# Kernel optimization log

Hardware: AMD Instinct MI355X
Metric: run time of the kernel (lower is better)

## Reference

```python
import jax, jax.numpy as jnp
import numpy as np

# Correlation hyperparameters (from init_kwargs):
PAD = 4            # pad_size
KERNEL = 1         # kernel_size (point-wise)
MD = 4             # max_displacement
STRIDE1 = 1
STRIDE2 = 1

B, C, H, W = 8, 256, 96, 160


def setup_inputs() -> dict:
    key = jax.random.key(0)
    k1, k2 = jax.random.split(key)
    input1 = jax.random.normal(k1, (B, C, H, W), dtype=jnp.float32)
    input2 = jax.random.normal(k2, (B, C, H, W), dtype=jnp.float32)
    return {"input1": input1, "input2": input2}


def reference(input1, input2):
    """FlowNet-style correlation cost volume.

    out[b, (dy+MD)*D + (dx+MD), y, x] = (1/C) * sum_c in1[b,c,y,x] * in2pad[b,c,y+dy+PAD, x+dx+PAD]
    where in2pad is input2 zero-padded by PAD and D = 2*MD+1. With PAD == MD,
    kernel_size == 1, stride1 == stride2 == 1 the output is [B, D*D, H, W].
    """
    b, c, h, w = input1.shape
    in2p = jnp.pad(input2, ((0, 0), (0, 0), (PAD, PAD), (PAD, PAD)))
    D = 2 * MD + 1
    outs = []
    # Fixed small 81-iteration loop over displacements (not a data dim).
    for dy in range(0, 2 * MD + 1, STRIDE2):
        for dx in range(0, 2 * MD + 1, STRIDE2):
            shifted = jax.lax.dynamic_slice(in2p, (0, 0, dy, dx), (b, c, h, w))
            # mean over channels == sum / (kernel^2 * C) with kernel == 1
            outs.append(jnp.mean(input1 * shifted, axis=1))
    return jnp.stack(outs, axis=1)  # [B, 81, H, W]
```

## Files before the change

### kernel.cpp

```cpp
#include <hip/hip_runtime.h>
#include <stdint.h>

#define B_ 8
#define C_ 256
#define H_ 96
#define W_ 160
#define ND 9
#define NDISP 81
#define NCHUNK 128
#define TX 4
#define NXG 20
#define NTHR 256
#define NCOMP 180
#define IN2_OFF 320
#define ROW_B 352
#define BUF_B 3584
#define NBUF 4
#define NSEG 218
#define HW (H_ * W_)
#define CHSTEP (2 * HW)

typedef __attribute__((ext_vector_type(2))) _Float16 half2v;

__device__ __forceinline__ unsigned pk(float lo, float hi) {
    return __builtin_bit_cast(unsigned, __builtin_amdgcn_cvt_pkrtz(lo, hi));
}
__device__ __forceinline__ float dot2acc(unsigned a, unsigned w, float acc) {
#if __has_builtin(__builtin_amdgcn_fdot2)
    return __builtin_amdgcn_fdot2(__builtin_bit_cast(half2v, a),
                                  __builtin_bit_cast(half2v, w), acc, false);
#else
    half2v av = __builtin_bit_cast(half2v, a);
    half2v wv = __builtin_bit_cast(half2v, w);
    return acc + (float)av.x * (float)wv.x + (float)av.y * (float)wv.y;
#endif
}

__device__ __forceinline__ const float* seg_src(int s, int b, int y, int h,
        const float* in1, const float* in2, int* woff)
{
    if (s < 20) {
        *woff = s * 16;
        return in1 + ((size_t)(b * C_) * H_ + y) * W_ + 80 * h + 4 * s;
    }
    const int t = s - 20;
    const int r = t / 22, k = t - r * 22;
    *woff = IN2_OFF + r * ROW_B + k * 16;
    int row = y + r - 4;
    row = row < 0 ? 0 : (row >= H_ ? H_ - 1 : row);
    int x = 80 * h - 4 + 4 * k;
    x = x < 0 ? 0 : (x > W_ - 4 ? W_ - 4 : x);
    return in2 + ((size_t)(b * C_) * H_ + row) * W_ + x;
}

__global__ __launch_bounds__(NTHR) void corr_hx16_kernel(
    const float* __restrict__ in1,
    const float* __restrict__ in2,
    float* __restrict__ out)
{
    __shared__ __align__(16) unsigned lds[NBUF * BUF_B / 4];

    const int tid = threadIdx.x;
    const int b   = blockIdx.x & 7;
    const int idx = blockIdx.x >> 3;
    const int y   = idx >> 1;
    const int h   = idx & 1;

    int w0off = 0;
    const bool v0 = tid < NSEG;
    const float* p0 = in1;
    if (v0) p0 = seg_src(tid, b, y, h, in1, in2, &w0off);

    const bool isComp = (tid < NCOMP);
    const int  dy = isComp ? (tid / NXG) : 0;
    const int  xg = isComp ? (tid % NXG) : 0;
    const int  x0 = 80 * h + TX * xg;
    const bool rowOk = (y + dy - 4 >= 0) && (y + dy - 4 < H_);
    const bool mzW0 = (h == 0) && (xg == 0);
    const bool mzW2 = (h == 1) && (xg == NXG - 1);

    const int aof = 16 * xg;
    const int wof = IN2_OFF + dy * ROW_B + 16 * xg;

    float acc[ND][TX];
    #pragma unroll
    for (int dx = 0; dx < ND; ++dx)
        #pragma unroll
        for (int j = 0; j < TX; ++j) acc[dx][j] = 0.f;

    float4 SAp0, SAp1;
    float4 SBp0, SBp1;

    #define LOADS(S) do {                                                     \
        S##p0 = *(const float4*)(p0);  S##p1 = *(const float4*)(p0 + HW);     \
        p0 += CHSTEP;                                                         \
    } while (0);

    #define CVTW(BUFI, S) do {                                                \
        if (v0) {                                                             \
            char* base = (char*)lds + (BUFI) * BUF_B;                         \
            *(uint4*)(base + w0off) = make_uint4(                             \
                pk(S##p0.x, S##p1.x), pk(S##p0.y, S##p1.y),                   \
                pk(S##p0.z, S##p1.z), pk(S##p0.w, S##p1.w));                  \
        }                                                                     \
    } while (0);

    #define COMPUTE(BUFI)                                                     \
    if (isComp) {                                                             \
        const char* bb = (const char*)lds + (BUFI) * BUF_B;                   \
        uint4 A0 = *(const uint4*)(bb + aof);                                 \
        uint4 W0 = *(const uint4*)(bb + wof);                                 \
        uint4 W1 = *(const uint4*)(bb + wof + 16);                            \
        uint4 W2 = *(const uint4*)(bb + wof + 32);                            \
        if (mzW0) W0 = make_uint4(0u, 0u, 0u, 0u);                            \
        if (mzW2) W2 = make_uint4(0u, 0u, 0u, 0u);                            \
        unsigned a[4]  = {A0.x, A0.y, A0.z, A0.w};                            \
        unsigned w[12] = {W0.x, W0.y, W0.z, W0.w, W1.x, W1.y, W1.z, W1.w,     \
                          W2.x, W2.y, W2.z, W2.w};                            \
        _Pragma("unroll")                                                     \
        for (int dx = 0; dx < ND; ++dx) {                                     \
            _Pragma("unroll")                                                 \
            for (int j = 0; j < TX; ++j)                                      \
                acc[dx][j] = dot2acc(a[j], w[dx + j], acc[dx][j]);            \
        }                                                                     \
    }

    #define BODY(KM4, SWR, SLD, DOW, DOL)                                     \
        if (DOW) { CVTW(((KM4) + 2) & 3, SWR) }                               \
        if (DOL) { LOADS(SLD) }                                               \
        COMPUTE(KM4)                                                          \
        __syncthreads();

    LOADS(SA)
    CVTW(0, SA)
    LOADS(SA)
    CVTW(1, SA)
    LOADS(SB)
    __syncthreads();

    #pragma unroll 1
    for (int g = 0; g < 31; ++g) {
        BODY(0, SB, SA, true, true)
        BODY(1, SA, SB, true, true)
        BODY(2, SB, SA, true, true)
        BODY(3, SA, SB, true, true)
    }
    BODY(0, SB, SA, true, true)
    BODY(1, SA, SB, true, false)
    BODY(2, SA, SA, false, false)
    BODY(3, SA, SA, false, false)

    #undef BODY
    #undef COMPUTE
    #undef CVTW
    #undef LOADS

    if (isComp) {
        const float m = rowOk ? (1.0f / (float)C_) : 0.f;
        float* outp = out + ((size_t)(b * NDISP + dy * ND) * H_ + y) * W_ + x0;
        #pragma unroll
        for (int dx = 0; dx < ND; ++dx) {
            float4 o = make_float4(acc[dx][0] * m, acc[dx][1] * m,
                                   acc[dx][2] * m, acc[dx][3] * m);
            *(float4*)(outp + dx * HW) = o;
        }
    }
}

extern "C" void kernel_launch(void* const* d_in, const int* in_sizes, int n_in,
                              void* d_out, int out_size, void* d_ws, size_t ws_size,
                              hipStream_t stream) {
    const float* in1 = (const float*)d_in[0];
    const float* in2 = (const float*)d_in[1];
    float* out = (float*)d_out;

    const int grid = B_ * H_ * 2;
    corr_hx16_kernel<<<grid, NTHR, 0, stream>>>(in1, in2, out);
}
```

Measured before the change: 111.1 us.

## Process four channels per pipeline stage with a triple-buffered LDS ring

Each stage now loads four channels instead of two, packs them as two fp16 pairs into one larger LDS buffer, and computes both pairs before a barrier. The ring shrinks from four buffers to three, with one register set in place of two alternating sets. This halves the number of __syncthreads and loop iterations and puts more loads in flight per stage. In exchange each stage is longer, the lookahead is shallower, and the extra float4 registers may raise register pressure.

```diff
diff --git a/kernel.cpp b/kernel.cpp
--- a/kernel.cpp
+++ b/kernel.cpp
@@ -7,18 +7,19 @@
 #define W_ 160
 #define ND 9
 #define NDISP 81
-#define NCHUNK 128
+#define NCHUNK 64
 #define TX 4
 #define NXG 20
 #define NTHR 256
 #define NCOMP 180
 #define IN2_OFF 320
 #define ROW_B 352
-#define BUF_B 3584
-#define NBUF 4
+#define PAIR_B 3520
+#define BUF_B 7040
+#define NBUF 3
 #define NSEG 218
 #define HW (H_ * W_)
-#define CHSTEP (2 * HW)
+#define CHSTEP (4 * HW)
 
 typedef __attribute__((ext_vector_type(2))) _Float16 half2v;
 
@@ -53,7 +54,7 @@
     return in2 + ((size_t)(b * C_) * H_ + row) * W_ + x;
 }
 
-__global__ __launch_bounds__(NTHR) void corr_hx16_kernel(
+__global__ __launch_bounds__(NTHR) void corr_ck4_kernel(
     const float* __restrict__ in1,
     const float* __restrict__ in2,
     float* __restrict__ out)
@@ -88,30 +89,33 @@
         #pragma unroll
         for (int j = 0; j < TX; ++j) acc[dx][j] = 0.f;
 
-    float4 SAp0, SAp1;
-    float4 SBp0, SBp1;
+    float4 SAp0, SAp1, SAq0, SAq1;
 
-    #define LOADS(S) do {                                                     \
-        S##p0 = *(const float4*)(p0);  S##p1 = *(const float4*)(p0 + HW);     \
+    #define LOADS do {                                                        \
+        SAp0 = *(const float4*)(p0);                        \
+        SAp1 = *(const float4*)(p0 + HW);                   \
+        SAq0 = *(const float4*)(p0 + 2 * HW);               \
+        SAq1 = *(const float4*)(p0 + 3 * HW);               \
         p0 += CHSTEP;                                                         \
     } while (0);
 
-    #define CVTW(BUFI, S) do {                                                \
+    #define CVTW(BUFI) do {                                                   \
         if (v0) {                                                             \
-            char* base = (char*)lds + (BUFI) * BUF_B;                         \
-            *(uint4*)(base + w0off) = make_uint4(                             \
-                pk(S##p0.x, S##p1.x), pk(S##p0.y, S##p1.y),                   \
-                pk(S##p0.z, S##p1.z), pk(S##p0.w, S##p1.w));                  \
+            char* base = (char*)lds + (BUFI) * BUF_B + w0off;                 \
+            *(uint4*)(base) = make_uint4(                                     \
+                pk(SAp0.x, SAp1.x), pk(SAp0.y, SAp1.y),                       \
+                pk(SAp0.z, SAp1.z), pk(SAp0.w, SAp1.w));                      \
+            *(uint4*)(base + PAIR_B) = make_uint4(                            \
+                pk(SAq0.x, SAq1.x), pk(SAq0.y, SAq1.y),                       \
+                pk(SAq0.z, SAq1.z), pk(SAq0.w, SAq1.w));                      \
         }                                                                     \
     } while (0);
 
-    #define COMPUTE(BUFI)                                                     \
-    if (isComp) {                                                             \
-        const char* bb = (const char*)lds + (BUFI) * BUF_B;                   \
-        uint4 A0 = *(const uint4*)(bb + aof);                                 \
-        uint4 W0 = *(const uint4*)(bb + wof);                                 \
-        uint4 W1 = *(const uint4*)(bb + wof + 16);                            \
-        uint4 W2 = *(const uint4*)(bb + wof + 32);                            \
+    #define FPAIR(BB) {                                                       \
+        uint4 A0 = *(const uint4*)((BB) + aof);                               \
+        uint4 W0 = *(const uint4*)((BB) + wof);                               \
+        uint4 W1 = *(const uint4*)((BB) + wof + 16);                          \
+        uint4 W2 = *(const uint4*)((BB) + wof + 32);                          \
         if (mzW0) W0 = make_uint4(0u, 0u, 0u, 0u);                            \
         if (mzW2) W2 = make_uint4(0u, 0u, 0u, 0u);                            \
         unsigned a[4]  = {A0.x, A0.y, A0.z, A0.w};                            \
@@ -125,33 +129,38 @@
         }                                                                     \
     }
 
-    #define BODY(KM4, SWR, SLD, DOW, DOL)                                     \
-        if (DOW) { CVTW(((KM4) + 2) & 3, SWR) }                               \
-        if (DOL) { LOADS(SLD) }                                               \
-        COMPUTE(KM4)                                                          \
+    #define COMPUTE(BUFI)                                                     \
+    if (isComp) {                                                             \
+        const char* bb = (const char*)lds + (BUFI) * BUF_B;                   \
+        FPAIR(bb)                                                             \
+        FPAIR(bb + PAIR_B)                                                    \
+    }
+
+    #define BODY(BUFC, BUFW, DOW, DOL)                                        \
+        if (DOW) { CVTW(BUFW) }                                               \
+        if (DOL) { LOADS }                                                    \
+        COMPUTE(BUFC)                                                         \
         __syncthreads();
 
-    LOADS(SA)
-    CVTW(0, SA)
-    LOADS(SA)
-    CVTW(1, SA)
-    LOADS(SB)
+    LOADS
+    CVTW(0)
+    LOADS
     __syncthreads();
 
     #pragma unroll 1
-    for (int g = 0; g < 31; ++g) {
-        BODY(0, SB, SA, true, true)
-        BODY(1, SA, SB, true, true)
-        BODY(2, SB, SA, true, true)
-        BODY(3, SA, SB, true, true)
+    for (int g = 0; g < 20; ++g) {
+        BODY(0, 1, true, true)
+        BODY(1, 2, true, true)
+        BODY(2, 0, true, true)
     }
-    BODY(0, SB, SA, true, true)
-    BODY(1, SA, SB, true, false)
-    BODY(2, SA, SA, false, false)
-    BODY(3, SA, SA, false, false)
+    BODY(0, 1, true, true)
+    BODY(1, 2, true, true)
+    BODY(2, 0, true, false)
+    BODY(0, 1, false, false)
 
     #undef BODY
     #undef COMPUTE
+    #undef FPAIR
     #undef CVTW
     #undef LOADS
 
@@ -175,5 +184,5 @@
     float* out = (float*)d_out;
 
     const int grid = B_ * H_ * 2;
-    corr_hx16_kernel<<<grid, NTHR, 0, stream>>>(in1, in2, out);
+    corr_ck4_kernel<<<grid, NTHR, 0, stream>>>(in1, in2, out);
 }
```

Result: slower. 121.6 us (+9.5%).
